# Kernel optimization log

Measured on AMD Instinct MI355X. Metric: run time of the kernel, lower is better.

Reference implementation:

```python
import jax, jax.numpy as jnp
import numpy as np

DIM = 1024
B, K = 8192, 16


def setup_inputs() -> dict:
    key = jax.random.key(0)
    ks = jax.random.split(key, 7)
    # xavier_uniform bound for square [C,C]: sqrt(6/(C+C))
    bq = float(np.sqrt(6.0 / (DIM + DIM)))
    ba_bound = float(np.sqrt(6.0 / (DIM + 1)))
    return {
        "query": jax.random.normal(ks[0], (B, DIM), dtype=jnp.float32),
        "key": jax.random.normal(ks[1], (B, K, DIM), dtype=jnp.float32),
        "value": jax.random.normal(ks[2], (B, K, DIM), dtype=jnp.float32),
        "Wq": jax.random.uniform(ks[3], (DIM, DIM), jnp.float32, -bq, bq),
        "Wk": jax.random.uniform(ks[4], (DIM, DIM), jnp.float32, -bq, bq),
        "Wa": jax.random.uniform(ks[5], (1, DIM), jnp.float32, -ba_bound, ba_bound),
        "ba": jnp.ones((1,), dtype=jnp.float32),
    }


def reference(query, key, value, Wq, Wk, Wa, ba):
    # query: [B, C]; key/value: [B, K, C]
    C = query.shape[-1]
    res = query
    q = query[:, None, :]                       # [B, 1, C]
    k = jnp.concatenate([q, key], axis=1)       # [B, K+1, C] (query prepended)
    v = jnp.concatenate([q, value], axis=1)     # [B, K+1, C]
    qp = q @ Wq.T                               # [B, 1, C]
    kp = k @ Wk.T                               # [B, K+1, C]
    scale = 1.0 / jnp.sqrt(jnp.asarray(C, dtype=jnp.float32))
    scores = jnp.einsum('bqc,bkc->bqk', qp, kp) * scale   # [B, 1, K+1]
    attn_w = jax.nn.softmax(scores, axis=-1)
    attn = jnp.einsum('bqk,bkc->bqc', attn_w, v)[:, 0, :]  # [B, C]
    alpha = jax.nn.sigmoid(res @ Wa.T + ba)     # [B, 1]
    out = res + alpha * attn                    # gated residual
    # F.normalize(p=2, dim=-1, eps=1e-12)
    norm = jnp.linalg.norm(out, axis=-1, keepdims=True)
    return out / jnp.maximum(norm, 1e-12)
```

## Files before the change

kernel.cpp:

```cpp
#include <hip/hip_runtime.h>
#include <hip/hip_bf16.h>

#define DIM   1024
#define BATCH 8192
#define KV    16

typedef __attribute__((ext_vector_type(4))) float f32x4;
typedef __attribute__((ext_vector_type(8))) short short8;

static __device__ __forceinline__ unsigned short f2bf(float x) {
  return __builtin_bit_cast(unsigned short, __float2bfloat16(x));
}

static __device__ __forceinline__ void gl_lds16(const unsigned short* g, unsigned short* l) {
  __builtin_amdgcn_global_load_lds(
      (const __attribute__((address_space(1))) void*)g,
      (__attribute__((address_space(3))) void*)l, 16, 0, 0);
}

__global__ __launch_bounds__(256) void convert_q(const float4* __restrict__ in,
                                                 ushort4* __restrict__ out, int n4) {
  int i = blockIdx.x * blockDim.x + threadIdx.x;
  int stride = gridDim.x * blockDim.x;
  for (; i < n4; i += stride) {
    float4 f = in[i];
    ushort4 o;
    o.x = f2bf(f.x); o.y = f2bf(f.y); o.z = f2bf(f.z); o.w = f2bf(f.w);
    out[i] = o;
  }
}

__global__ __launch_bounds__(256) void transpose_w(const float* __restrict__ Wq,
                                                   const float* __restrict__ Wk,
                                                   unsigned short* __restrict__ WqT,
                                                   unsigned short* __restrict__ WkT) {
  __shared__ float tile[32][33];
  const float* src = blockIdx.z ? Wk : Wq;
  unsigned short* dst = blockIdx.z ? WkT : WqT;
  int x = blockIdx.x * 32 + threadIdx.x;
  int y0 = blockIdx.y * 32;
  #pragma unroll
  for (int i = threadIdx.y; i < 32; i += 8)
    tile[i][threadIdx.x] = src[(size_t)(y0 + i) * DIM + x];
  __syncthreads();
  int x2 = blockIdx.y * 32 + threadIdx.x;
  int y2 = blockIdx.x * 32;
  #pragma unroll
  for (int i = threadIdx.y; i < 32; i += 8)
    dst[(size_t)(y2 + i) * DIM + x2] = f2bf(tile[threadIdx.x][i]);
}

template<int BF16OUT>
__global__ __launch_bounds__(256) void gemm_nt(const unsigned short* __restrict__ A,
                                               const unsigned short* __restrict__ B,
                                               void* __restrict__ Cv,
                                               int M, int N, int K) {
  __shared__ __align__(16) unsigned short As[128 * 32];
  __shared__ __align__(16) unsigned short Bs[128 * 32];
  const int tid  = threadIdx.x;
  const int lane = tid & 63;
  const int wave = tid >> 6;
  const int wr = wave >> 1, wc = wave & 1;
  const size_t bm = (size_t)blockIdx.x * 128;
  const size_t bn = (size_t)blockIdx.y * 128;

  f32x4 acc[4][4];
  #pragma unroll
  for (int m = 0; m < 4; ++m)
    #pragma unroll
    for (int n = 0; n < 4; ++n)
      acc[m][n] = (f32x4){0.f, 0.f, 0.f, 0.f};

  const int r0 = tid >> 2;
  const int r1 = 64 + (tid >> 2);
  const int cc = (tid & 3) * 8;
  const int kg = lane >> 4;
  const int rowf = lane & 15;

  for (int kt = 0; kt < K; kt += 32) {
    gl_lds16(A + (bm + r0) * K + kt + cc, As + tid * 8);
    gl_lds16(A + (bm + r1) * K + kt + cc, As + 2048 + tid * 8);
    gl_lds16(B + (bn + r0) * K + kt + cc, Bs + tid * 8);
    gl_lds16(B + (bn + r1) * K + kt + cc, Bs + 2048 + tid * 8);
    __syncthreads();
    short8 af[4], bfr[4];
    #pragma unroll
    for (int m = 0; m < 4; ++m)
      af[m] = *(const short8*)(As + ((wr * 64 + m * 16 + rowf) * 32 + kg * 8));
    #pragma unroll
    for (int n = 0; n < 4; ++n)
      bfr[n] = *(const short8*)(Bs + ((wc * 64 + n * 16 + rowf) * 32 + kg * 8));
    #pragma unroll
    for (int m = 0; m < 4; ++m)
      #pragma unroll
      for (int n = 0; n < 4; ++n)
        acc[m][n] = __builtin_amdgcn_mfma_f32_16x16x32_bf16(af[m], bfr[n], acc[m][n], 0, 0, 0);
    __syncthreads();
  }

  const int rq = (lane >> 4) * 4;
  const int colf = lane & 15;
  #pragma unroll
  for (int m = 0; m < 4; ++m)
    #pragma unroll
    for (int n = 0; n < 4; ++n)
      #pragma unroll
      for (int i = 0; i < 4; ++i) {
        size_t row = bm + wr * 64 + m * 16 + rq + i;
        size_t col = bn + wc * 64 + n * 16 + colf;
        if (BF16OUT)
          ((unsigned short*)Cv)[row * N + col] = f2bf(acc[m][n][i]);
        else
          ((float*)Cv)[row * N + col] = acc[m][n][i];
      }
}

__global__ __launch_bounds__(256) void epilogue(const float* __restrict__ query,
                                                const float* __restrict__ key,
                                                const float* __restrict__ value,
                                                const float* __restrict__ Wa,
                                                const float* __restrict__ ba,
                                                const float* __restrict__ u,
                                                float* __restrict__ out) {
  const int b = blockIdx.x;
  const int tid = threadIdx.x;
  const int lane = tid & 63, wave = tid >> 6;
  const float4* q4 = (const float4*)(query + (size_t)b * DIM);
  const float4* u4 = (const float4*)(u + (size_t)b * DIM);
  const float4* k4 = (const float4*)(key + (size_t)b * KV * DIM);
  const float4* v4 = (const float4*)(value + (size_t)b * KV * DIM);

  float4 qv = q4[tid];
  float4 uv = u4[tid];
  float4 wv = ((const float4*)Wa)[tid];

  float s[17];
  s[0] = qv.x * uv.x + qv.y * uv.y + qv.z * uv.z + qv.w * uv.w;
  float ad = qv.x * wv.x + qv.y * wv.y + qv.z * wv.z + qv.w * wv.w;
  #pragma unroll
  for (int j = 1; j <= 16; ++j) {
    float4 kv = k4[(j - 1) * 256 + tid];
    s[j] = uv.x * kv.x + uv.y * kv.y + uv.z * kv.z + uv.w * kv.w;
  }

  #pragma unroll
  for (int m = 32; m >= 1; m >>= 1) {
    #pragma unroll
    for (int j = 0; j < 17; ++j) s[j] += __shfl_xor(s[j], m);
    ad += __shfl_xor(ad, m);
  }
  __shared__ float red[4][18];
  if (lane == 0) {
    #pragma unroll
    for (int j = 0; j < 17; ++j) red[wave][j] = s[j];
    red[wave][17] = ad;
  }
  __syncthreads();

  float wt[17];
  float mx = -1e30f;
  #pragma unroll
  for (int j = 0; j < 17; ++j) {
    float t = (red[0][j] + red[1][j] + red[2][j] + red[3][j]) * 0.03125f;
    wt[j] = t;
    mx = fmaxf(mx, t);
  }
  float den = 0.f;
  #pragma unroll
  for (int j = 0; j < 17; ++j) {
    wt[j] = expf(wt[j] - mx);
    den += wt[j];
  }
  float adt = red[0][17] + red[1][17] + red[2][17] + red[3][17] + ba[0];
  float alpha = 1.0f / (1.0f + expf(-adt));
  float am = alpha / den;

  float4 acc;
  acc.x = wt[0] * qv.x; acc.y = wt[0] * qv.y; acc.z = wt[0] * qv.z; acc.w = wt[0] * qv.w;
  #pragma unroll
  for (int j = 1; j <= 16; ++j) {
    float4 vv = v4[(j - 1) * 256 + tid];
    acc.x += wt[j] * vv.x; acc.y += wt[j] * vv.y;
    acc.z += wt[j] * vv.z; acc.w += wt[j] * vv.w;
  }
  float4 t;
  t.x = qv.x + am * acc.x; t.y = qv.y + am * acc.y;
  t.z = qv.z + am * acc.z; t.w = qv.w + am * acc.w;

  float ssp = t.x * t.x + t.y * t.y + t.z * t.z + t.w * t.w;
  #pragma unroll
  for (int m = 32; m >= 1; m >>= 1) ssp += __shfl_xor(ssp, m);
  __shared__ float red2[4];
  if (lane == 0) red2[wave] = ssp;
  __syncthreads();
  float nrm = sqrtf(red2[0] + red2[1] + red2[2] + red2[3]);
  float inv = 1.0f / fmaxf(nrm, 1e-12f);

  float4 o;
  o.x = t.x * inv; o.y = t.y * inv; o.z = t.z * inv; o.w = t.w * inv;
  ((float4*)(out + (size_t)b * DIM))[tid] = o;
}

extern "C" void kernel_launch(void* const* d_in, const int* in_sizes, int n_in,
                              void* d_out, int out_size, void* d_ws, size_t ws_size,
                              hipStream_t stream) {
  const float* query = (const float*)d_in[0];
  const float* key   = (const float*)d_in[1];
  const float* value = (const float*)d_in[2];
  const float* Wq    = (const float*)d_in[3];
  const float* Wk    = (const float*)d_in[4];
  const float* Wa    = (const float*)d_in[5];
  const float* ba    = (const float*)d_in[6];

  unsigned short* qbf = (unsigned short*)d_ws;
  unsigned short* WqT = qbf + (size_t)BATCH * DIM;
  unsigned short* WkT = WqT + (size_t)DIM * DIM;
  unsigned short* Mt  = WkT + (size_t)DIM * DIM;

  convert_q<<<2048, 256, 0, stream>>>((const float4*)query, (ushort4*)qbf, BATCH * DIM / 4);
  transpose_w<<<dim3(32, 32, 2), dim3(32, 8), 0, stream>>>(Wq, Wk, WqT, WkT);
  gemm_nt<1><<<dim3(8, 8), 256, 0, stream>>>(WkT, WqT, Mt, DIM, DIM, DIM);
  gemm_nt<0><<<dim3(BATCH / 128, DIM / 128), 256, 0, stream>>>(qbf, Mt, d_out, BATCH, DIM, DIM);
  epilogue<<<BATCH, 256, 0, stream>>>(query, key, value, Wa, ba,
                                      (const float*)d_out, (float*)d_out);
}
```

Before: 287.1 us.

## Store u in bf16, retile weight GEMM, swizzle grid, prefetch V nontemporally

The small Wk^T·Wq GEMM now uses 64x64 tiles so 256 workgroups cover the device instead of 64. The big u GEMM writes bf16 into the first half of each output row, with a row stride of 2048 shorts, and uses a 1D grid remapped across groups of eight. The epilogue reads u as bf16, loads all 16 value rows up front alongside the key loads using nontemporal hints, and uses vector arithmetic. The aim is to cut GEMM write traffic and idle CUs, and to overlap V loads with the score reductions, at the cost of extra register pressure and bf16 rounding of u.

```diff
diff --git a/kernel.cpp b/kernel.cpp
--- a/kernel.cpp
+++ b/kernel.cpp
@@ -10,6 +10,12 @@
 
 static __device__ __forceinline__ unsigned short f2bf(float x) {
   return __builtin_bit_cast(unsigned short, __float2bfloat16(x));
+}
+static __device__ __forceinline__ float bf2f(unsigned short x) {
+  return __bfloat162float(__builtin_bit_cast(__hip_bfloat16, x));
+}
+static __device__ __forceinline__ float dot4(f32x4 a, f32x4 b) {
+  return a.x * b.x + a.y * b.y + a.z * b.z + a.w * b.w;
 }
 
 static __device__ __forceinline__ void gl_lds16(const unsigned short* g, unsigned short* l) {
@@ -18,12 +24,12 @@
       (__attribute__((address_space(3))) void*)l, 16, 0, 0);
 }
 
-__global__ __launch_bounds__(256) void convert_q(const float4* __restrict__ in,
+__global__ __launch_bounds__(256) void convert_q(const f32x4* __restrict__ in,
                                                  ushort4* __restrict__ out, int n4) {
   int i = blockIdx.x * blockDim.x + threadIdx.x;
   int stride = gridDim.x * blockDim.x;
   for (; i < n4; i += stride) {
-    float4 f = in[i];
+    f32x4 f = in[i];
     ushort4 o;
     o.x = f2bf(f.x); o.y = f2bf(f.y); o.z = f2bf(f.z); o.w = f2bf(f.w);
     out[i] = o;
@@ -50,19 +56,77 @@
     dst[(size_t)(y2 + i) * DIM + x2] = f2bf(tile[threadIdx.x][i]);
 }
 
-template<int BF16OUT>
-__global__ __launch_bounds__(256) void gemm_nt(const unsigned short* __restrict__ A,
-                                               const unsigned short* __restrict__ B,
-                                               void* __restrict__ Cv,
-                                               int M, int N, int K) {
-  __shared__ __align__(16) unsigned short As[128 * 32];
-  __shared__ __align__(16) unsigned short Bs[128 * 32];
-  const int tid  = threadIdx.x;
+__global__ __launch_bounds__(256) void gemm_nt64(const unsigned short* __restrict__ A,
+                                                 const unsigned short* __restrict__ B,
+                                                 unsigned short* __restrict__ C,
+                                                 int N, int K) {
+  __shared__ __align__(16) unsigned short As[64 * 32];
+  __shared__ __align__(16) unsigned short Bs[64 * 32];
+  const int tid = threadIdx.x;
   const int lane = tid & 63;
   const int wave = tid >> 6;
   const int wr = wave >> 1, wc = wave & 1;
-  const size_t bm = (size_t)blockIdx.x * 128;
-  const size_t bn = (size_t)blockIdx.y * 128;
+  const size_t bm = (size_t)blockIdx.x * 64;
+  const size_t bn = (size_t)blockIdx.y * 64;
+
+  f32x4 acc[2][2];
+  #pragma unroll
+  for (int m = 0; m < 2; ++m)
+    #pragma unroll
+    for (int n = 0; n < 2; ++n)
+      acc[m][n] = (f32x4){0.f, 0.f, 0.f, 0.f};
+
+  const int r0 = tid >> 2;
+  const int cc = (tid & 3) * 8;
+  const int kg = lane >> 4;
+  const int rowf = lane & 15;
+
+  for (int kt = 0; kt < K; kt += 32) {
+    gl_lds16(A + (bm + r0) * K + kt + cc, As + tid * 8);
+    gl_lds16(B + (bn + r0) * K + kt + cc, Bs + tid * 8);
+    __syncthreads();
+    short8 af[2], bfr[2];
+    #pragma unroll
+    for (int m = 0; m < 2; ++m)
+      af[m] = *(const short8*)(As + ((wr * 32 + m * 16 + rowf) * 32 + kg * 8));
+    #pragma unroll
+    for (int n = 0; n < 2; ++n)
+      bfr[n] = *(const short8*)(Bs + ((wc * 32 + n * 16 + rowf) * 32 + kg * 8));
+    #pragma unroll
+    for (int m = 0; m < 2; ++m)
+      #pragma unroll
+      for (int n = 0; n < 2; ++n)
+        acc[m][n] = __builtin_amdgcn_mfma_f32_16x16x32_bf16(af[m], bfr[n], acc[m][n], 0, 0, 0);
+    __syncthreads();
+  }
+
+  const int rq = (lane >> 4) * 4;
+  const int colf = lane & 15;
+  #pragma unroll
+  for (int m = 0; m < 2; ++m)
+    #pragma unroll
+    for (int n = 0; n < 2; ++n)
+      #pragma unroll
+      for (int i = 0; i < 4; ++i)
+        C[(bm + wr * 32 + m * 16 + rq + i) * N + bn + wc * 32 + n * 16 + colf] =
+            f2bf(acc[m][n][i]);
+}
+
+__global__ __launch_bounds__(256) void gemm_u(const unsigned short* __restrict__ A,
+                                              const unsigned short* __restrict__ B,
+                                              unsigned short* __restrict__ C,
+                                              int K, int ntN, int ldc) {
+  const int cpx = gridDim.x >> 3;
+  const int wg = (blockIdx.x & 7) * cpx + (blockIdx.x >> 3);
+  const size_t bm = (size_t)(wg / ntN) * 128;
+  const size_t bn = (size_t)(wg % ntN) * 128;
+
+  __shared__ __align__(16) unsigned short As[128 * 32];
+  __shared__ __align__(16) unsigned short Bs[128 * 32];
+  const int tid = threadIdx.x;
+  const int lane = tid & 63;
+  const int wave = tid >> 6;
+  const int wr = wave >> 1, wc = wave & 1;
 
   f32x4 acc[4][4];
   #pragma unroll
@@ -108,10 +172,7 @@
       for (int i = 0; i < 4; ++i) {
         size_t row = bm + wr * 64 + m * 16 + rq + i;
         size_t col = bn + wc * 64 + n * 16 + colf;
-        if (BF16OUT)
-          ((unsigned short*)Cv)[row * N + col] = f2bf(acc[m][n][i]);
-        else
-          ((float*)Cv)[row * N + col] = acc[m][n][i];
+        C[row * (size_t)ldc + col] = f2bf(acc[m][n][i]);
       }
 }
 
@@ -120,28 +181,34 @@
                                                 const float* __restrict__ value,
                                                 const float* __restrict__ Wa,
                                                 const float* __restrict__ ba,
-                                                const float* __restrict__ u,
+                                                const unsigned short* __restrict__ u,
                                                 float* __restrict__ out) {
   const int b = blockIdx.x;
   const int tid = threadIdx.x;
   const int lane = tid & 63, wave = tid >> 6;
-  const float4* q4 = (const float4*)(query + (size_t)b * DIM);
-  const float4* u4 = (const float4*)(u + (size_t)b * DIM);
-  const float4* k4 = (const float4*)(key + (size_t)b * KV * DIM);
-  const float4* v4 = (const float4*)(value + (size_t)b * KV * DIM);
-
-  float4 qv = q4[tid];
-  float4 uv = u4[tid];
-  float4 wv = ((const float4*)Wa)[tid];
+  const f32x4* q4 = (const f32x4*)(query + (size_t)b * DIM);
+  const f32x4* k4 = (const f32x4*)(key + (size_t)b * KV * DIM);
+  const f32x4* v4 = (const f32x4*)(value + (size_t)b * KV * DIM);
+
+  f32x4 qv = q4[tid];
+  ushort4 ub = ((const ushort4*)(u + (size_t)b * 2048))[tid];
+  f32x4 uv;
+  uv.x = bf2f(ub.x); uv.y = bf2f(ub.y); uv.z = bf2f(ub.z); uv.w = bf2f(ub.w);
+  f32x4 wv = ((const f32x4*)Wa)[tid];
 
   float s[17];
-  s[0] = qv.x * uv.x + qv.y * uv.y + qv.z * uv.z + qv.w * uv.w;
-  float ad = qv.x * wv.x + qv.y * wv.y + qv.z * wv.z + qv.w * wv.w;
+  s[0] = dot4(qv, uv);
+  float ad = dot4(qv, wv);
   #pragma unroll
   for (int j = 1; j <= 16; ++j) {
-    float4 kv = k4[(j - 1) * 256 + tid];
-    s[j] = uv.x * kv.x + uv.y * kv.y + uv.z * kv.z + uv.w * kv.w;
-  }
+    f32x4 kv = __builtin_nontemporal_load(k4 + (j - 1) * 256 + tid);
+    s[j] = dot4(uv, kv);
+  }
+
+  f32x4 vv[16];
+  #pragma unroll
+  for (int j = 0; j < 16; ++j)
+    vv[j] = __builtin_nontemporal_load(v4 + j * 256 + tid);
 
   #pragma unroll
   for (int m = 32; m >= 1; m >>= 1) {
@@ -175,19 +242,12 @@
   float alpha = 1.0f / (1.0f + expf(-adt));
   float am = alpha / den;
 
-  float4 acc;
-  acc.x = wt[0] * qv.x; acc.y = wt[0] * qv.y; acc.z = wt[0] * qv.z; acc.w = wt[0] * qv.w;
-  #pragma unroll
-  for (int j = 1; j <= 16; ++j) {
-    float4 vv = v4[(j - 1) * 256 + tid];
-    acc.x += wt[j] * vv.x; acc.y += wt[j] * vv.y;
-    acc.z += wt[j] * vv.z; acc.w += wt[j] * vv.w;
-  }
-  float4 t;
-  t.x = qv.x + am * acc.x; t.y = qv.y + am * acc.y;
-  t.z = qv.z + am * acc.z; t.w = qv.w + am * acc.w;
-
-  float ssp = t.x * t.x + t.y * t.y + t.z * t.z + t.w * t.w;
+  f32x4 acc = qv * wt[0];
+  #pragma unroll
+  for (int j = 1; j <= 16; ++j) acc += vv[j - 1] * wt[j];
+  f32x4 t = qv + acc * am;
+
+  float ssp = dot4(t, t);
   #pragma unroll
   for (int m = 32; m >= 1; m >>= 1) ssp += __shfl_xor(ssp, m);
   __shared__ float red2[4];
@@ -196,9 +256,7 @@
   float nrm = sqrtf(red2[0] + red2[1] + red2[2] + red2[3]);
   float inv = 1.0f / fmaxf(nrm, 1e-12f);
 
-  float4 o;
-  o.x = t.x * inv; o.y = t.y * inv; o.z = t.z * inv; o.w = t.w * inv;
-  ((float4*)(out + (size_t)b * DIM))[tid] = o;
+  ((f32x4*)(out + (size_t)b * DIM))[tid] = t * inv;
 }
 
 extern "C" void kernel_launch(void* const* d_in, const int* in_sizes, int n_in,
@@ -216,11 +274,11 @@
   unsigned short* WqT = qbf + (size_t)BATCH * DIM;
   unsigned short* WkT = WqT + (size_t)DIM * DIM;
   unsigned short* Mt  = WkT + (size_t)DIM * DIM;
-
-  convert_q<<<2048, 256, 0, stream>>>((const float4*)query, (ushort4*)qbf, BATCH * DIM / 4);
+  unsigned short* ubf = (unsigned short*)d_out;
+
+  convert_q<<<2048, 256, 0, stream>>>((const f32x4*)query, (ushort4*)qbf, BATCH * DIM / 4);
   transpose_w<<<dim3(32, 32, 2), dim3(32, 8), 0, stream>>>(Wq, Wk, WqT, WkT);
-  gemm_nt<1><<<dim3(8, 8), 256, 0, stream>>>(WkT, WqT, Mt, DIM, DIM, DIM);
-  gemm_nt<0><<<dim3(BATCH / 128, DIM / 128), 256, 0, stream>>>(qbf, Mt, d_out, BATCH, DIM, DIM);
-  epilogue<<<BATCH, 256, 0, stream>>>(query, key, value, Wa, ba,
-                                      (const float*)d_out, (float*)d_out);
-}
+  gemm_nt64<<<dim3(16, 16), 256, 0, stream>>>(WkT, WqT, Mt, DIM, DIM);
+  gemm_u<<<512, 256, 0, stream>>>(qbf, Mt, ubf, DIM, DIM / 128, 2048);
+  epilogue<<<BATCH, 256, 0, stream>>>(query, key, value, Wa, ba, ubf, (float*)d_out);
+}
```

New measurement: 245.6 us. 14.5% less time.
